# Optimization experiments

Measured on AMD Instinct MI355X. Metric: run time of the kernel, lower is better.

The kernel has to match this reference:

```python
import jax, jax.numpy as jnp
import numpy as np

D, NH, NL, NP, DFF = 256, 8, 4, 4, 1024
DH = D // NH
SHAPES = [(64, 64), (32, 32), (16, 16), (8, 8)]
LEN = sum(h * w for h, w in SHAPES)  # 5440
B = 4
EPS = 1e-5


def setup_inputs() -> dict:
    key = jax.random.key(0)
    ks = jax.random.split(key, 24)
    def lin_w(k, fin, fout, scale=None):
        s = (1.0 / np.sqrt(fin)) if scale is None else scale
        return jax.random.normal(k, (fin, fout), jnp.float32) * s
    def lin_b(k, fout, scale=0.01):
        return jax.random.normal(k, (fout,), jnp.float32) * scale
    inp = {
        'src': jax.random.normal(ks[0], (B, LEN, D), jnp.float32),
        'pos_lvl_embed': jax.random.normal(ks[1], (B, LEN, D), jnp.float32),
        'spatial_shapes': jnp.array(SHAPES, jnp.int32),
        'level_start_index': jnp.array(np.cumsum([0] + [h * w for h, w in SHAPES[:-1]]), jnp.int32),
        # MSDeformAttn params
        'Wv': lin_w(ks[2], D, D), 'bv': lin_b(ks[3], D),
        'Woff': lin_w(ks[4], D, NH * NL * NP * 2, scale=0.001),  # small offsets, like grid init
        'boff': jax.random.normal(ks[5], (NH * NL * NP * 2,), jnp.float32) * 0.5,
        'Wa': lin_w(ks[6], D, NH * NL * NP), 'ba': lin_b(ks[7], NH * NL * NP),
        'Wo': lin_w(ks[8], D, D), 'bo': lin_b(ks[9], D),
        # FFN params
        'W1': lin_w(ks[10], D, DFF), 'b1': lin_b(ks[11], DFF),
        'W2': lin_w(ks[12], DFF, D), 'b2': lin_b(ks[13], D),
        # LayerNorms
        'g1': jnp.ones((D,), jnp.float32), 'be1': jnp.zeros((D,), jnp.float32),
        'g2': jnp.ones((D,), jnp.float32), 'be2': jnp.zeros((D,), jnp.float32),
    }
    return inp


def _layernorm(x, g, b):
    mu = jnp.mean(x, axis=-1, keepdims=True)
    var = jnp.var(x, axis=-1, keepdims=True)
    return (x - mu) * jax.lax.rsqrt(var + EPS) * g + b


def _bilinear(v, x, y):
    # v: [B, H, W, NH, DH]; x, y: [B, Lq, NH, NP] pixel coords (align_corners=False, zero padding)
    Bv, H, W = v.shape[0], v.shape[1], v.shape[2]
    x0, y0 = jnp.floor(x), jnp.floor(y)
    bb = jnp.arange(Bv)[:, None, None, None]
    hh = jnp.arange(NH)[None, None, :, None]
    out = 0.0
    for dx in (0, 1):
        for dy in (0, 1):
            xi, yi = x0 + dx, y0 + dy
            w = (1.0 - jnp.abs(x - xi)) * (1.0 - jnp.abs(y - yi))
            valid = (xi >= 0) & (xi <= W - 1) & (yi >= 0) & (yi <= H - 1)
            xc = jnp.clip(xi, 0, W - 1).astype(jnp.int32)
            yc = jnp.clip(yi, 0, H - 1).astype(jnp.int32)
            out = out + v[bb, yc, xc, hh] * (w * valid)[..., None]
    return out  # [B, Lq, NH, NP, DH]


def _ms_deform_attn(query, value_flat, shapes, starts, Wv, bv, Woff, boff, Wa, ba, Wo, bo):
    Bq, Lq = query.shape[0], query.shape[1]
    # reference points: normalized center of each query's own spatial location (valid_ratios == 1)
    refs = []
    for (H, W) in shapes:
        gy, gx = jnp.meshgrid(jnp.arange(H, dtype=jnp.float32), jnp.arange(W, dtype=jnp.float32), indexing='ij')
        refs.append(jnp.stack([(gx + 0.5) / W, (gy + 0.5) / H], -1).reshape(-1, 2))
    ref = jnp.concatenate(refs, 0)  # [Len, 2] (x, y)

    value = (value_flat @ Wv + bv).reshape(Bq, Lq, NH, DH)
    off = (query @ Woff + boff).reshape(Bq, Lq, NH, NL, NP, 2)
    attn = jax.nn.softmax((query @ Wa + ba).reshape(Bq, Lq, NH, NL * NP), axis=-1).reshape(Bq, Lq, NH, NL, NP)
    norm = jnp.array([[w, h] for (h, w) in shapes], jnp.float32)  # [NL, 2] = (W, H)
    loc = ref[None, :, None, None, None, :] + off / norm[None, None, None, :, None, :]  # [B,Lq,NH,NL,NP,2]

    out = 0.0
    for l, (H, W) in enumerate(shapes):
        s = starts[l]
        v_l = value[:, s:s + H * W].reshape(Bq, H, W, NH, DH)
        x = loc[:, :, :, l, :, 0] * W - 0.5
        y = loc[:, :, :, l, :, 1] * H - 0.5
        sampled = _bilinear(v_l, x, y)  # [B,Lq,NH,NP,DH]
        out = out + jnp.sum(sampled * attn[:, :, :, l, :, None], axis=3)
    return out.reshape(Bq, Lq, D) @ Wo + bo


def reference(src, spatial_shapes, level_start_index, pos_lvl_embed,
              Wv, bv, Woff, boff, Wa, ba, Wo, bo,
              W1, b1, W2, b2, g1, be1, g2, be2):
    shapes = [(int(h), int(w)) for h, w in np.asarray(spatial_shapes)]  # static metadata
    starts = [int(s) for s in np.asarray(level_start_index)]
    src2 = _ms_deform_attn(src + pos_lvl_embed, src, shapes, starts, Wv, bv, Woff, boff, Wa, ba, Wo, bo)
    x = _layernorm(src + src2, g1, be1)
    ffn = jax.nn.relu(x @ W1 + b1) @ W2 + b2
    return _layernorm(x + ffn, g2, be2)
```

## Files before the change

kernel.cpp:

```cpp
#include <hip/hip_runtime.h>
#include <hip/hip_fp16.h>
#include <cstddef>
#include <cstdint>

#define DMODEL 256
#define NHEAD  8
#define NLVL   4
#define NPT    4
#define DHEAD  32
#define DFFN   1024
#define SLEN   5440
#define BATCH  4
#define NTOK   (BATCH * SLEN)
#define NT256  ((size_t)NTOK * 256)
#define GYR    170
#define GYP    176
#define LN_EPS 1e-5f

typedef __attribute__((ext_vector_type(4))) float f32x4;
typedef __attribute__((ext_vector_type(8))) short s16x8;

__device__ __forceinline__ unsigned short f2bf(float f) {
    union { float f; unsigned u; } v; v.f = f;
    unsigned u = v.u;
    u += 0x7FFFu + ((u >> 16) & 1u);
    return (unsigned short)(u >> 16);
}
__device__ __forceinline__ float bf2f(unsigned short h) {
    union { unsigned u; float f; } v; v.u = ((unsigned)h) << 16;
    return v.f;
}

__device__ __forceinline__ void g2l16(const unsigned short* g, unsigned short* l) {
    __builtin_amdgcn_global_load_lds(
        (const __attribute__((address_space(1))) unsigned int*)g,
        (__attribute__((address_space(3))) unsigned int*)l, 16, 0, 0);
}

__global__ __launch_bounds__(256) void prep_kernel(
    const float* __restrict__ src, const float* __restrict__ pos,
    unsigned short* __restrict__ srcB, unsigned short* __restrict__ qB)
{
    const size_t i = ((size_t)blockIdx.x * 256 + threadIdx.x) * 4;
    const float4 s = *(const float4*)(src + i);
    const float4 p = *(const float4*)(pos + i);
    ushort4 sb, qb;
    sb.x = f2bf(s.x); sb.y = f2bf(s.y); sb.z = f2bf(s.z); sb.w = f2bf(s.w);
    qb.x = f2bf(s.x + p.x); qb.y = f2bf(s.y + p.y);
    qb.z = f2bf(s.z + p.z); qb.w = f2bf(s.w + p.w);
    *(ushort4*)(srcB + i) = sb;
    *(ushort4*)(qB + i) = qb;
}

__global__ __launch_bounds__(256) void transpose_all_kernel(
    const float* __restrict__ Wv, const float* __restrict__ Woff,
    const float* __restrict__ Wa, const float* __restrict__ Wo,
    const float* __restrict__ W1, const float* __restrict__ W2,
    unsigned short* __restrict__ WvT, unsigned short* __restrict__ WcatT,
    unsigned short* __restrict__ WoT,
    unsigned short* __restrict__ W1T, unsigned short* __restrict__ W2T)
{
    const int bid = blockIdx.x;
    const float* W; unsigned short* Wt; int K, N, t;
    if (bid < 16)       { W = Wv;   Wt = WvT;              K = 256;  N = 256;  t = bid; }
    else if (bid < 32)  { W = Woff; Wt = WcatT;            K = 256;  N = 256;  t = bid - 16; }
    else if (bid < 40)  { W = Wa;   Wt = WcatT + 256*256;  K = 256;  N = 128;  t = bid - 32; }
    else if (bid < 56)  { W = Wo;   Wt = WoT;              K = 256;  N = 256;  t = bid - 40; }
    else if (bid < 120) { W = W1;   Wt = W1T;              K = 256;  N = 1024; t = bid - 56; }
    else                { W = W2;   Wt = W2T;              K = 1024; N = 256;  t = bid - 120; }
    const int ntx = N >> 6;
    const int k0 = (t / ntx) * 64, n0 = (t % ntx) * 64;

    __shared__ float T[64][65];
    const int r  = threadIdx.x >> 4;
    const int c4 = (threadIdx.x & 15) * 4;
    #pragma unroll
    for (int rep = 0; rep < 4; rep++) {
        const int k = rep * 16 + r;
        const float4 v = *(const float4*)(W + (size_t)(k0 + k) * N + n0 + c4);
        T[c4 + 0][k] = v.x; T[c4 + 1][k] = v.y;
        T[c4 + 2][k] = v.z; T[c4 + 3][k] = v.w;
    }
    __syncthreads();
    #pragma unroll
    for (int rep = 0; rep < 4; rep++) {
        const int n = rep * 16 + r;
        ushort4 o;
        o.x = f2bf(T[n][c4 + 0]); o.y = f2bf(T[n][c4 + 1]);
        o.z = f2bf(T[n][c4 + 2]); o.w = f2bf(T[n][c4 + 3]);
        *(ushort4*)(Wt + (size_t)(n0 + n) * K + k0 + c4) = o;
    }
}

template <int KK, int COLS, int NX, bool RELU, int OM>
__global__ __launch_bounds__(256, 4) void gemm_mk_kernel(
    const unsigned short* __restrict__ A,
    const unsigned short* __restrict__ Bt,
    const float* __restrict__ bias, const float* __restrict__ bias2,
    int bsplit,
    void* __restrict__ Cout, int N)
{
    const int lin = blockIdx.x;
    const int c8  = lin & 7;
    const int rr  = lin >> 3;
    const int bx  = rr % NX;
    const int yy  = (rr / NX) * 8 + c8;
    if (yy >= GYR) return;

    constexpr int LDB = KK + 8;
    __shared__ __align__(16) unsigned short sB[COLS * LDB];

    const int tid  = threadIdx.x;
    const int w    = tid >> 6;
    const int lane = tid & 63;
    const int m16  = lane & 15;
    const int q    = lane >> 4;
    const int col0 = bx * COLS;

    constexpr int K8  = KK / 8;
    constexpr int NCH = COLS * K8 / 256;
    #pragma unroll
    for (int c = 0; c < NCH; c++) {
        const int id = c * 256 + tid;
        const int bc = id / K8;
        const int k8 = id - bc * K8;
        *(int4*)&sB[bc * LDB + k8 * 8] =
            *(const int4*)(Bt + (size_t)(col0 + bc) * KK + k8 * 8);
    }
    __syncthreads();

    constexpr int NJ = COLS / 16;

    #pragma unroll
    for (int c = 0; c < 2; c++) {
        const int rowb = (yy * 2 + c) * 64 + w * 16;
        const unsigned short* ap = A + (size_t)(rowb + m16) * KK + q * 8;

        f32x4 acc[NJ];
        #pragma unroll
        for (int j = 0; j < NJ; j++) acc[j] = (f32x4){0.f, 0.f, 0.f, 0.f};

        #pragma unroll 8
        for (int ks = 0; ks < KK / 32; ks++) {
            const s16x8 af = *(const s16x8*)(ap + ks * 32);
            #pragma unroll
            for (int j = 0; j < NJ; j++) {
                const s16x8 bf = *(const s16x8*)
                    &sB[(j * 16 + m16) * LDB + ks * 32 + q * 8];
                acc[j] = __builtin_amdgcn_mfma_f32_16x16x32_bf16(
                    af, bf, acc[j], 0, 0, 0);
            }
        }

        #pragma unroll
        for (int j = 0; j < NJ; j++) {
            const int col = col0 + j * 16 + m16;
            const float bcol = (col < bsplit) ? bias[col] : bias2[col - bsplit];
            #pragma unroll
            for (int r = 0; r < 4; r++) {
                const int row = rowb + q * 4 + r;
                float v = acc[j][r] + bcol;
                if (RELU) v = fmaxf(v, 0.f);
                if (OM == 1)
                    ((unsigned short*)Cout)[(size_t)row * N + col] = f2bf(v);
                else if (OM == 2)
                    ((__half*)Cout)[(size_t)row * N + col] = __float2half(v);
                else
                    ((float*)Cout)[(size_t)row * N + col] = v;
            }
        }
    }
}

template <int KK, bool RELU, int OM>
__global__ __launch_bounds__(256, 2) void gemm_lds_kernel(
    const unsigned short* __restrict__ A,
    const unsigned short* __restrict__ Bt,
    const float* __restrict__ bias,
    void* __restrict__ Cout, int N)
{
    const int bid  = blockIdx.x;
    const int nbx  = N >> 7;
    const int by   = bid / nbx;
    const int bx   = bid - by * nbx;
    const int row0 = by * 128;
    const int col0 = bx * 128;

    __shared__ __align__(16) unsigned short sA[128 * 64];
    __shared__ __align__(16) unsigned short sB[128 * 64];

    const int tid  = threadIdx.x;
    const int wid  = tid >> 6;
    const int lane = tid & 63;
    const int m16  = lane & 15;
    const int q    = lane >> 4;
    const int wr   = (wid >> 1) * 64;
    const int wc   = (wid & 1) * 64;

    const int srow = lane >> 3;
    const int schk = (lane & 7) ^ srow;

    f32x4 acc[4][4];
    #pragma unroll
    for (int m = 0; m < 4; m++)
        #pragma unroll
        for (int n = 0; n < 4; n++) acc[m][n] = (f32x4){0.f, 0.f, 0.f, 0.f};

    #pragma unroll 1
    for (int kt = 0; kt < KK / 64; kt++) {
        #pragma unroll
        for (int i = 0; i < 4; i++) {
            const int j = wid * 4 + i;
            const int r = j * 8 + srow;
            g2l16(A  + (size_t)(row0 + r) * KK + kt * 64 + schk * 8, &sA[j * 512]);
            g2l16(Bt + (size_t)(col0 + r) * KK + kt * 64 + schk * 8, &sB[j * 512]);
        }
        __syncthreads();

        #pragma unroll
        for (int ks = 0; ks < 2; ks++) {
            s16x8 a[4], b[4];
            #pragma unroll
            for (int m = 0; m < 4; m++) {
                const int r  = wr + m * 16 + m16;
                const int cc = (ks * 4 + q) ^ (r & 7);
                a[m] = *(const s16x8*)&sA[r * 64 + cc * 8];
            }
            #pragma unroll
            for (int n = 0; n < 4; n++) {
                const int r  = wc + n * 16 + m16;
                const int cc = (ks * 4 + q) ^ (r & 7);
                b[n] = *(const s16x8*)&sB[r * 64 + cc * 8];
            }
            #pragma unroll
            for (int m = 0; m < 4; m++)
                #pragma unroll
                for (int n = 0; n < 4; n++)
                    acc[m][n] = __builtin_amdgcn_mfma_f32_16x16x32_bf16(
                        a[m], b[n], acc[m][n], 0, 0, 0);
        }
        __syncthreads();
    }

    #pragma unroll
    for (int n = 0; n < 4; n++) {
        const int col  = col0 + wc + n * 16 + m16;
        const float bc = bias[col];
        #pragma unroll
        for (int m = 0; m < 4; m++) {
            #pragma unroll
            for (int r = 0; r < 4; r++) {
                const int row = row0 + wr + m * 16 + q * 4 + r;
                float v = acc[m][n][r] + bc;
                if (RELU) v = fmaxf(v, 0.f);
                if (OM == 1)
                    ((unsigned short*)Cout)[(size_t)row * N + col] = f2bf(v);
                else if (OM == 2)
                    ((__half*)Cout)[(size_t)row * N + col] = __float2half(v);
                else
                    ((float*)Cout)[(size_t)row * N + col] = v;
            }
        }
    }
}

__global__ __launch_bounds__(256) void msda_meta_kernel(
    const float* __restrict__ olg, uint4* __restrict__ meta)
{
    const int t  = blockIdx.x * 256 + threadIdx.x;
    const int p  = t & 15;
    const int h  = (t >> 4) & 7;
    const int bq = t >> 7;
    const int b  = bq / SLEN;
    const int q  = bq - b * SLEN;

    int rem, Wq;
    if (q < 4096)      { rem = q;        Wq = 64; }
    else if (q < 5120) { rem = q - 4096; Wq = 32; }
    else if (q < 5376) { rem = q - 5120; Wq = 16; }
    else               { rem = q - 5376; Wq = 8;  }
    const int gy = rem / Wq;
    const int gx = rem - gy * Wq;
    const float ref_x = (gx + 0.5f) / (float)Wq;
    const float ref_y = (gy + 0.5f) / (float)Wq;

    const float lg = olg[(size_t)bq * 384 + 256 + h * 16 + p];
    float mx = lg;
    #pragma unroll
    for (int m = 1; m < 16; m <<= 1) mx = fmaxf(mx, __shfl_xor(mx, m));
    const float e = expf(lg - mx);
    float s = e;
    #pragma unroll
    for (int m = 1; m < 16; m <<= 1) s += __shfl_xor(s, m);
    const float aw = e / s;

    const float2 o2 = *(const float2*)(olg + (size_t)bq * 384 + h * 32 + 2 * p);

    const int l = p >> 2;
    constexpr int LW[4] = {64, 32, 16, 8};
    constexpr int LS[4] = {0, 4096, 5120, 5376};
    const int Wl = LW[l];
    const float fW = (float)Wl;

    const float X = (ref_x + o2.x / fW) * fW - 0.5f;
    const float Y = (ref_y + o2.y / fW) * fW - 0.5f;
    const float x0f = floorf(X), y0f = floorf(Y);
    const float fx = X - x0f, fy = Y - y0f;
    const int x0 = (int)x0f, y0 = (int)y0f;

    unsigned idx[4]; __half hw[4];
    #pragma unroll
    for (int dy = 0; dy < 2; dy++) {
        const int yi = y0 + dy;
        const float wy = dy ? fy : (1.f - fy);
        const bool vy = (yi >= 0) && (yi < Wl);
        const int yc = min(max(yi, 0), Wl - 1);
        #pragma unroll
        for (int dx = 0; dx < 2; dx++) {
            const int xi = x0 + dx;
            const float wx = dx ? fx : (1.f - fx);
            const bool vx = (xi >= 0) && (xi < Wl);
            const int xc = min(max(xi, 0), Wl - 1);
            const int c = dy * 2 + dx;
            idx[c] = (unsigned)(LS[l] + yc * Wl + xc);
            hw[c] = __float2half((vx && vy) ? (aw * wx * wy) : 0.f);
        }
    }
    union { __half2 h2; unsigned u; } pk0, pk1;
    pk0.h2 = __halves2half2(hw[0], hw[1]);
    pk1.h2 = __halves2half2(hw[2], hw[3]);
    uint4 m;
    m.x = idx[0] | (idx[1] << 16);
    m.y = idx[2] | (idx[3] << 16);
    m.z = pk0.u;
    m.w = pk1.u;
    meta[((size_t)bq * 16 + p) * 8 + h] = m;
}

__global__ __launch_bounds__(256) void msda_sample_kernel(
    const __half* __restrict__ value, const uint4* __restrict__ meta,
    unsigned short* __restrict__ out)
{
    const int lin = blockIdx.x;
    const int c8  = lin & 7;
    const int rr  = lin >> 3;
    const int b   = c8 >> 1;
    const int i8  = (c8 & 1) + 2 * rr;

    const int tid = threadIdx.x;
    const int sub = tid & 3;
    const int h   = (tid >> 2) & 7;
    const int t8  = tid >> 5;
    const int bq  = b * SLEN + i8 * 8 + t8;

    const char* vb = (const char*)value + (size_t)b * SLEN * 512;
    const unsigned laneoff = (unsigned)(h * 64 + sub * 16);
    const uint4* metap = meta + (size_t)bq * 128 + h;

    __half2 acc[4][4];
    #pragma unroll
    for (int i = 0; i < 4; i++)
        #pragma unroll
        for (int k = 0; k < 4; k++)
            acc[i][k] = __float2half2_rn(0.f);

    for (int g = 0; g < 4; g++) {
        #pragma unroll
        for (int pp = 0; pp < 4; pp++) {
            const int p = g * 4 + pp;
            const uint4 m = metap[p * 8];
            const unsigned a0 = ((m.x & 0xFFFFu) << 9) + laneoff;
            const unsigned a1 = ((m.x >> 16) << 9) + laneoff;
            const unsigned a2 = ((m.y & 0xFFFFu) << 9) + laneoff;
            const unsigned a3 = ((m.y >> 16) << 9) + laneoff;
            const int4 v0 = *(const int4*)(vb + a0);
            const int4 v1 = *(const int4*)(vb + a1);
            const int4 v2 = *(const int4*)(vb + a2);
            const int4 v3 = *(const int4*)(vb + a3);
            union { unsigned u; __half2 h2; } wz, ww;
            wz.u = m.z; ww.u = m.w;
            const __half2 ws0 = __half2half2(__low2half(wz.h2));
            const __half2 ws1 = __half2half2(__high2half(wz.h2));
            const __half2 ws2 = __half2half2(__low2half(ww.h2));
            const __half2 ws3 = __half2half2(__high2half(ww.h2));
            const __half2* p0 = (const __half2*)&v0;
            const __half2* p1 = (const __half2*)&v1;
            const __half2* p2 = (const __half2*)&v2;
            const __half2* p3 = (const __half2*)&v3;
            #pragma unroll
            for (int k = 0; k < 4; k++) {
                acc[pp][k] = __hfma2(ws0, p0[k], acc[pp][k]);
                acc[pp][k] = __hfma2(ws1, p1[k], acc[pp][k]);
                acc[pp][k] = __hfma2(ws2, p2[k], acc[pp][k]);
                acc[pp][k] = __hfma2(ws3, p3[k], acc[pp][k]);
            }
        }
    }

    uint4 o;
    unsigned* ou = &o.x;
    #pragma unroll
    for (int k = 0; k < 4; k++) {
        float2 s = {0.f, 0.f};
        #pragma unroll
        for (int i = 0; i < 4; i++) {
            const float2 f = __half22float2(acc[i][k]);
            s.x += f.x; s.y += f.y;
        }
        ou[k] = (unsigned)f2bf(s.x) | ((unsigned)f2bf(s.y) << 16);
    }
    *(uint4*)(out + (size_t)bq * 256 + h * 32 + sub * 8) = o;
}

template <bool X1B, bool X2B, bool WF, bool WB>
__global__ __launch_bounds__(256) void ln_kernel(
    const void* __restrict__ x1, const void* __restrict__ x2,
    const float* __restrict__ g, const float* __restrict__ be,
    float* __restrict__ outf, unsigned short* __restrict__ outb)
{
    const int lane = threadIdx.x & 63;
    const int wid  = threadIdx.x >> 6;
    const size_t row  = (size_t)blockIdx.x * 4 + wid;
    const size_t base = row * 256 + lane * 4;

    float a0, a1, a2, a3, b0, b1, b2, b3;
    if (X1B) {
        const ushort4 a = *(const ushort4*)((const unsigned short*)x1 + base);
        a0 = bf2f(a.x); a1 = bf2f(a.y); a2 = bf2f(a.z); a3 = bf2f(a.w);
    } else {
        const float4 a = *(const float4*)((const float*)x1 + base);
        a0 = a.x; a1 = a.y; a2 = a.z; a3 = a.w;
    }
    if (X2B) {
        const ushort4 b = *(const ushort4*)((const unsigned short*)x2 + base);
        b0 = bf2f(b.x); b1 = bf2f(b.y); b2 = bf2f(b.z); b3 = bf2f(b.w);
    } else {
        const float4 b = *(const float4*)((const float*)x2 + base);
        b0 = b.x; b1 = b.y; b2 = b.z; b3 = b.w;
    }
    const float v0 = a0 + b0, v1 = a1 + b1, v2 = a2 + b2, v3 = a3 + b3;

    float s  = v0 + v1 + v2 + v3;
    float s2 = v0 * v0 + v1 * v1 + v2 * v2 + v3 * v3;
    #pragma unroll
    for (int o = 32; o > 0; o >>= 1) {
        s  += __shfl_xor(s, o);
        s2 += __shfl_xor(s2, o);
    }
    const float mu  = s * (1.f / 256.f);
    const float var = s2 * (1.f / 256.f) - mu * mu;
    const float r   = rsqrtf(var + LN_EPS);

    const float4 gv = *(const float4*)(g  + lane * 4);
    const float4 bv = *(const float4*)(be + lane * 4);
    float4 o4;
    o4.x = (v0 - mu) * r * gv.x + bv.x;
    o4.y = (v1 - mu) * r * gv.y + bv.y;
    o4.z = (v2 - mu) * r * gv.z + bv.z;
    o4.w = (v3 - mu) * r * gv.w + bv.w;
    if (WF) *(float4*)(outf + base) = o4;
    if (WB) {
        ushort4 ob;
        ob.x = f2bf(o4.x); ob.y = f2bf(o4.y); ob.z = f2bf(o4.z); ob.w = f2bf(o4.w);
        *(ushort4*)(outb + base) = ob;
    }
}

extern "C" void kernel_launch(void* const* d_in, const int* in_sizes, int n_in,
                              void* d_out, int out_size, void* d_ws, size_t ws_size,
                              hipStream_t stream)
{
    const float* src  = (const float*)d_in[0];
    const float* pos  = (const float*)d_in[1];
    const float* Wv   = (const float*)d_in[4];
    const float* bv   = (const float*)d_in[5];
    const float* Woff = (const float*)d_in[6];
    const float* boff = (const float*)d_in[7];
    const float* Wa   = (const float*)d_in[8];
    const float* ba   = (const float*)d_in[9];
    const float* Wo   = (const float*)d_in[10];
    const float* bo   = (const float*)d_in[11];
    const float* W1   = (const float*)d_in[12];
    const float* b1   = (const float*)d_in[13];
    const float* W2   = (const float*)d_in[14];
    const float* b2   = (const float*)d_in[15];
    const float* g1   = (const float*)d_in[16];
    const float* be1  = (const float*)d_in[17];
    const float* g2   = (const float*)d_in[18];
    const float* be2  = (const float*)d_in[19];
    float* out = (float*)d_out;

    char* wsp = (char*)d_ws;
    unsigned short* srcB = (unsigned short*)wsp; wsp += NT256 * 2;
    unsigned short* qB   = (unsigned short*)wsp; wsp += NT256 * 2;
    unsigned short* tbufB = srcB;
    __half*         valB = (__half*)wsp;         wsp += NT256 * 2;
    float*          olg  = (float*)wsp;          wsp += (size_t)NTOK * 384 * 4;
    float*          src2 = olg;
    unsigned short* aoB  = (unsigned short*)wsp; wsp += NT256 * 2;
    unsigned short* xB   = (unsigned short*)wsp; wsp += NT256 * 2;
    unsigned short* h    = (unsigned short*)wsp; wsp += (size_t)NTOK * 1024 * 2;
    uint4*          meta = (uint4*)h;
    unsigned short* WvT  = (unsigned short*)wsp; wsp += 256 * 256 * 2;
    unsigned short* WcatT= (unsigned short*)wsp; wsp += 384 * 256 * 2;
    unsigned short* WoT  = (unsigned short*)wsp; wsp += 256 * 256 * 2;
    unsigned short* W1T  = (unsigned short*)wsp; wsp += 1024 * 256 * 2;
    unsigned short* W2T  = (unsigned short*)wsp; wsp += 256 * 1024 * 2;

    const dim3 blk(256);

    prep_kernel<<<dim3(NT256 / 1024), blk, 0, stream>>>(src, pos, srcB, qB);
    transpose_all_kernel<<<dim3(184), blk, 0, stream>>>(
        Wv, Woff, Wa, Wo, W1, W2, WvT, WcatT, WoT, W1T, W2T);

    gemm_mk_kernel<256, 64, 4, false, 2><<<dim3(4 * GYP), blk, 0, stream>>>(
        srcB, WvT, bv, bv, 1 << 30, valB, 256);
    gemm_mk_kernel<256, 64, 6, false, 0><<<dim3(6 * GYP), blk, 0, stream>>>(
        qB, WcatT, boff, ba, 256, olg, 384);
    msda_meta_kernel<<<dim3(NTOK * 128 / 256), blk, 0, stream>>>(olg, meta);
    msda_sample_kernel<<<dim3(NTOK / 8), blk, 0, stream>>>(valB, meta, aoB);
    gemm_mk_kernel<256, 64, 4, false, 0><<<dim3(4 * GYP), blk, 0, stream>>>(
        aoB, WoT, bo, bo, 1 << 30, src2, 256);
    ln_kernel<false, false, false, true><<<dim3(NTOK / 4), blk, 0, stream>>>(
        src, src2, g1, be1, nullptr, xB);
    gemm_mk_kernel<256, 64, 16, true, 1><<<dim3(16 * GYP), blk, 0, stream>>>(
        xB, W1T, b1, b1, 1 << 30, h, 1024);
    gemm_lds_kernel<1024, false, 1><<<dim3(340), blk, 0, stream>>>(
        h, W2T, b2, tbufB, 256);
    ln_kernel<true, true, true, false><<<dim3(NTOK / 4), blk, 0, stream>>>(
        xB, tbufB, g2, be2, out, nullptr);
}
```

Before: 275.0 us.

## Use 128x128 LDS-tiled GEMM for all projections and fuse prep with weight transpose

Drops the streaming-A gemm_mk kernel and sends every projection GEMM (value, offsets/attn, output, FFN1, FFN2) through the 128x128 LDS-tiled MFMA kernel. That kernel gains a split bias and the grouped block ordering. The activation bf16 prep and the weight transpose kernels are merged into one launch. The aim is more reuse of A and B tiles from LDS and one fewer launch, at the cost of lower occupancy (2 blocks per CU) and fewer blocks for the narrow GEMMs.

```diff
diff --git a/kernel.cpp b/kernel.cpp
--- a/kernel.cpp
+++ b/kernel.cpp
@@ -37,22 +37,9 @@
         (__attribute__((address_space(3))) unsigned int*)l, 16, 0, 0);
 }
 
-__global__ __launch_bounds__(256) void prep_kernel(
+__global__ __launch_bounds__(256) void prep_tr_kernel(
     const float* __restrict__ src, const float* __restrict__ pos,
-    unsigned short* __restrict__ srcB, unsigned short* __restrict__ qB)
-{
-    const size_t i = ((size_t)blockIdx.x * 256 + threadIdx.x) * 4;
-    const float4 s = *(const float4*)(src + i);
-    const float4 p = *(const float4*)(pos + i);
-    ushort4 sb, qb;
-    sb.x = f2bf(s.x); sb.y = f2bf(s.y); sb.z = f2bf(s.z); sb.w = f2bf(s.w);
-    qb.x = f2bf(s.x + p.x); qb.y = f2bf(s.y + p.y);
-    qb.z = f2bf(s.z + p.z); qb.w = f2bf(s.w + p.w);
-    *(ushort4*)(srcB + i) = sb;
-    *(ushort4*)(qB + i) = qb;
-}
-
-__global__ __launch_bounds__(256) void transpose_all_kernel(
+    unsigned short* __restrict__ srcB, unsigned short* __restrict__ qB,
     const float* __restrict__ Wv, const float* __restrict__ Woff,
     const float* __restrict__ Wa, const float* __restrict__ Wo,
     const float* __restrict__ W1, const float* __restrict__ W2,
@@ -60,7 +47,19 @@
     unsigned short* __restrict__ WoT,
     unsigned short* __restrict__ W1T, unsigned short* __restrict__ W2T)
 {
-    const int bid = blockIdx.x;
+    if (blockIdx.x < 5440) {
+        const size_t i = ((size_t)blockIdx.x * 256 + threadIdx.x) * 4;
+        const float4 s = *(const float4*)(src + i);
+        const float4 p = *(const float4*)(pos + i);
+        ushort4 sb, qb;
+        sb.x = f2bf(s.x); sb.y = f2bf(s.y); sb.z = f2bf(s.z); sb.w = f2bf(s.w);
+        qb.x = f2bf(s.x + p.x); qb.y = f2bf(s.y + p.y);
+        qb.z = f2bf(s.z + p.z); qb.w = f2bf(s.w + p.w);
+        *(ushort4*)(srcB + i) = sb;
+        *(ushort4*)(qB + i) = qb;
+        return;
+    }
+    const int bid = blockIdx.x - 5440;
     const float* W; unsigned short* Wt; int K, N, t;
     if (bid < 16)       { W = Wv;   Wt = WvT;              K = 256;  N = 256;  t = bid; }
     else if (bid < 32)  { W = Woff; Wt = WcatT;            K = 256;  N = 256;  t = bid - 16; }
@@ -92,8 +91,8 @@
     }
 }
 
-template <int KK, int COLS, int NX, bool RELU, int OM>
-__global__ __launch_bounds__(256, 4) void gemm_mk_kernel(
+template <int KK, int NXB, bool RELU, int OM>
+__global__ __launch_bounds__(256, 2) void gemm_lds_kernel(
     const unsigned short* __restrict__ A,
     const unsigned short* __restrict__ Bt,
     const float* __restrict__ bias, const float* __restrict__ bias2,
@@ -103,87 +102,10 @@
     const int lin = blockIdx.x;
     const int c8  = lin & 7;
     const int rr  = lin >> 3;
-    const int bx  = rr % NX;
-    const int yy  = (rr / NX) * 8 + c8;
+    const int bx  = rr % NXB;
+    const int yy  = (rr / NXB) * 8 + c8;
     if (yy >= GYR) return;
-
-    constexpr int LDB = KK + 8;
-    __shared__ __align__(16) unsigned short sB[COLS * LDB];
-
-    const int tid  = threadIdx.x;
-    const int w    = tid >> 6;
-    const int lane = tid & 63;
-    const int m16  = lane & 15;
-    const int q    = lane >> 4;
-    const int col0 = bx * COLS;
-
-    constexpr int K8  = KK / 8;
-    constexpr int NCH = COLS * K8 / 256;
-    #pragma unroll
-    for (int c = 0; c < NCH; c++) {
-        const int id = c * 256 + tid;
-        const int bc = id / K8;
-        const int k8 = id - bc * K8;
-        *(int4*)&sB[bc * LDB + k8 * 8] =
-            *(const int4*)(Bt + (size_t)(col0 + bc) * KK + k8 * 8);
-    }
-    __syncthreads();
-
-    constexpr int NJ = COLS / 16;
-
-    #pragma unroll
-    for (int c = 0; c < 2; c++) {
-        const int rowb = (yy * 2 + c) * 64 + w * 16;
-        const unsigned short* ap = A + (size_t)(rowb + m16) * KK + q * 8;
-
-        f32x4 acc[NJ];
-        #pragma unroll
-        for (int j = 0; j < NJ; j++) acc[j] = (f32x4){0.f, 0.f, 0.f, 0.f};
-
-        #pragma unroll 8
-        for (int ks = 0; ks < KK / 32; ks++) {
-            const s16x8 af = *(const s16x8*)(ap + ks * 32);
-            #pragma unroll
-            for (int j = 0; j < NJ; j++) {
-                const s16x8 bf = *(const s16x8*)
-                    &sB[(j * 16 + m16) * LDB + ks * 32 + q * 8];
-                acc[j] = __builtin_amdgcn_mfma_f32_16x16x32_bf16(
-                    af, bf, acc[j], 0, 0, 0);
-            }
-        }
-
-        #pragma unroll
-        for (int j = 0; j < NJ; j++) {
-            const int col = col0 + j * 16 + m16;
-            const float bcol = (col < bsplit) ? bias[col] : bias2[col - bsplit];
-            #pragma unroll
-            for (int r = 0; r < 4; r++) {
-                const int row = rowb + q * 4 + r;
-                float v = acc[j][r] + bcol;
-                if (RELU) v = fmaxf(v, 0.f);
-                if (OM == 1)
-                    ((unsigned short*)Cout)[(size_t)row * N + col] = f2bf(v);
-                else if (OM == 2)
-                    ((__half*)Cout)[(size_t)row * N + col] = __float2half(v);
-                else
-                    ((float*)Cout)[(size_t)row * N + col] = v;
-            }
-        }
-    }
-}
-
-template <int KK, bool RELU, int OM>
-__global__ __launch_bounds__(256, 2) void gemm_lds_kernel(
-    const unsigned short* __restrict__ A,
-    const unsigned short* __restrict__ Bt,
-    const float* __restrict__ bias,
-    void* __restrict__ Cout, int N)
-{
-    const int bid  = blockIdx.x;
-    const int nbx  = N >> 7;
-    const int by   = bid / nbx;
-    const int bx   = bid - by * nbx;
-    const int row0 = by * 128;
+    const int row0 = yy * 128;
     const int col0 = bx * 128;
 
     __shared__ __align__(16) unsigned short sA[128 * 64];
@@ -245,7 +167,7 @@
     #pragma unroll
     for (int n = 0; n < 4; n++) {
         const int col  = col0 + wc + n * 16 + m16;
-        const float bc = bias[col];
+        const float bc = (col < bsplit) ? bias[col] : bias2[col - bsplit];
         #pragma unroll
         for (int m = 0; m < 4; m++) {
             #pragma unroll
@@ -509,24 +431,24 @@
 
     const dim3 blk(256);
 
-    prep_kernel<<<dim3(NT256 / 1024), blk, 0, stream>>>(src, pos, srcB, qB);
-    transpose_all_kernel<<<dim3(184), blk, 0, stream>>>(
-        Wv, Woff, Wa, Wo, W1, W2, WvT, WcatT, WoT, W1T, W2T);
-
-    gemm_mk_kernel<256, 64, 4, false, 2><<<dim3(4 * GYP), blk, 0, stream>>>(
+    prep_tr_kernel<<<dim3(5624), blk, 0, stream>>>(
+        src, pos, srcB, qB, Wv, Woff, Wa, Wo, W1, W2,
+        WvT, WcatT, WoT, W1T, W2T);
+
+    gemm_lds_kernel<256, 2, false, 2><<<dim3(2 * GYP), blk, 0, stream>>>(
         srcB, WvT, bv, bv, 1 << 30, valB, 256);
-    gemm_mk_kernel<256, 64, 6, false, 0><<<dim3(6 * GYP), blk, 0, stream>>>(
+    gemm_lds_kernel<256, 3, false, 0><<<dim3(3 * GYP), blk, 0, stream>>>(
         qB, WcatT, boff, ba, 256, olg, 384);
     msda_meta_kernel<<<dim3(NTOK * 128 / 256), blk, 0, stream>>>(olg, meta);
     msda_sample_kernel<<<dim3(NTOK / 8), blk, 0, stream>>>(valB, meta, aoB);
-    gemm_mk_kernel<256, 64, 4, false, 0><<<dim3(4 * GYP), blk, 0, stream>>>(
+    gemm_lds_kernel<256, 2, false, 0><<<dim3(2 * GYP), blk, 0, stream>>>(
         aoB, WoT, bo, bo, 1 << 30, src2, 256);
     ln_kernel<false, false, false, true><<<dim3(NTOK / 4), blk, 0, stream>>>(
         src, src2, g1, be1, nullptr, xB);
-    gemm_mk_kernel<256, 64, 16, true, 1><<<dim3(16 * GYP), blk, 0, stream>>>(
+    gemm_lds_kernel<256, 8, true, 1><<<dim3(8 * GYP), blk, 0, stream>>>(
         xB, W1T, b1, b1, 1 << 30, h, 1024);
-    gemm_lds_kernel<1024, false, 1><<<dim3(340), blk, 0, stream>>>(
-        h, W2T, b2, tbufB, 256);
+    gemm_lds_kernel<1024, 2, false, 1><<<dim3(2 * GYP), blk, 0, stream>>>(
+        h, W2T, b2, b2, 1 << 30, tbufB, 256);
     ln_kernel<true, true, true, false><<<dim3(NTOK / 4), blk, 0, stream>>>(
         xB, tbufB, g2, be2, out, nullptr);
 }
```

After: 257.1 us. -6.5%, faster.
